# Kernel optimization log

Hardware: AMD Instinct MI355X
Metric: run time of the kernel (lower is better)

Reference implementation:

```python
import jax, jax.numpy as jnp
import numpy as np

RADIUS = 1.3
N_INTR = 128
STEP = 2.0 * RADIUS / N_INTR


def grid_sample_3d(vol, coords):
    # vol: [D,H,W,C]; coords: [N,3] as (x,y,z) in [-1,1]
    # Matches torch grid_sample(align_corners=True, mode='bilinear', padding_mode='border')
    D, H, W, C = vol.shape
    fx = jnp.clip((coords[:, 0] + 1.0) * 0.5 * (W - 1), 0.0, W - 1)
    fy = jnp.clip((coords[:, 1] + 1.0) * 0.5 * (H - 1), 0.0, H - 1)
    fz = jnp.clip((coords[:, 2] + 1.0) * 0.5 * (D - 1), 0.0, D - 1)
    x0 = jnp.floor(fx); y0 = jnp.floor(fy); z0 = jnp.floor(fz)
    wx = fx - x0; wy = fy - y0; wz = fz - z0
    x0i = x0.astype(jnp.int32); y0i = y0.astype(jnp.int32); z0i = z0.astype(jnp.int32)
    x1i = jnp.clip(x0i + 1, 0, W - 1)
    y1i = jnp.clip(y0i + 1, 0, H - 1)
    z1i = jnp.clip(z0i + 1, 0, D - 1)
    out = jnp.zeros((coords.shape[0], C), dtype=vol.dtype)
    for dz in (0, 1):
        iz = z0i if dz == 0 else z1i
        wgtz = (1.0 - wz) if dz == 0 else wz
        for dy in (0, 1):
            iy = y0i if dy == 0 else y1i
            wgty = (1.0 - wy) if dy == 0 else wy
            for dx in (0, 1):
                ix = x0i if dx == 0 else x1i
                wgtx = (1.0 - wx) if dx == 0 else wx
                out = out + vol[iz, iy, ix] * (wgtz * wgty * wgtx)[:, None]
    return out


def sh_deg4(d):
    # tcnn SphericalHarmonics degree 4: input (rd+1)/2, internally mapped back to rd.
    x, y, z = d[:, 0], d[:, 1], d[:, 2]
    x2, y2, z2 = x * x, y * y, z * z
    xy, yz, xz = x * y, y * z, x * z
    return jnp.stack([
        jnp.full_like(x, 0.28209479177387814),
        -0.48860251190291987 * y,
        0.48860251190291987 * z,
        -0.48860251190291987 * x,
        1.0925484305920792 * xy,
        -1.0925484305920792 * yz,
        0.94617469575755997 * z2 - 0.31539156525251999,
        -1.0925484305920792 * xz,
        0.54627421529603959 * (x2 - y2),
        0.59004358992664352 * y * (-3.0 * x2 + y2),
        2.8906114426405538 * xy * z,
        0.45704579946446572 * y * (1.0 - 5.0 * z2),
        0.3731763325901154 * z * (5.0 * z2 - 3.0),
        0.45704579946446572 * x * (1.0 - 5.0 * z2),
        1.4453057213202769 * z * (x2 - y2),
        0.59004358992664352 * x * (-x2 + 3.0 * y2),
    ], axis=-1)


def setup_inputs() -> dict:
    key = jax.random.key(0)
    ks = jax.random.split(key, 10)
    B = 8192
    return {
        'rays_o': jax.random.normal(ks[0], (B, 3), jnp.float32),
        'rays_d': jax.random.normal(ks[1], (B, 3), jnp.float32),
        'G1': 0.01 * jax.random.normal(ks[2], (256, 256, 256, 3), jnp.float32),
        'Fg': 0.05 * jax.random.normal(ks[3], (64, 64, 64, 32), jnp.float32),
        's_w0': 0.05 * jax.random.normal(ks[4], (32, 128), jnp.float32),
        's_w1': 0.05 * jax.random.normal(ks[5], (128, 128), jnp.float32),
        's_w2': 0.05 * jax.random.normal(ks[6], (128, 16), jnp.float32),
        'c_w0': 0.05 * jax.random.normal(ks[7], (31, 64), jnp.float32),
        'c_w1': 0.05 * jax.random.normal(ks[8], (64, 64), jnp.float32),
        'c_w2': 0.05 * jax.random.normal(ks[9], (64, 3), jnp.float32),
    }


def reference(rays_o, rays_d, G1, Fg, s_w0, s_w1, s_w2, c_w0, c_w1, c_w2):
    B = rays_o.shape[0]
    # ray / AABB [-R,R]^3 intersections with uniform stepping
    safe_d = jnp.where(jnp.abs(rays_d) < 1e-9, 1e-9, rays_d)
    t1 = (-RADIUS - rays_o) / safe_d
    t2 = (RADIUS - rays_o) / safe_d
    tmin = jnp.max(jnp.minimum(t1, t2), axis=-1)
    tmax = jnp.min(jnp.maximum(t1, t2), axis=-1)
    tnear = jnp.maximum(tmin, 0.0)
    ts = tnear[:, None] + jnp.arange(N_INTR + 1, dtype=jnp.float32) * STEP  # [B, N+1]
    mask = (ts[:, :-1] < tmax[:, None]) & (tmax > tnear)[:, None]  # [B, N]
    pts = rays_o[:, None, :] + rays_d[:, None, :] * ts[:, :-1, None]  # [B, N, 3]
    # forward scales pts to voxel coords then eval_pts maps back to [-1,1] => pts/RADIUS
    coords = (pts / RADIUS).reshape(-1, 3)
    g1 = grid_sample_3d(G1, coords)                 # [B*N, 3]  chained lookup
    fv = grid_sample_3d(Fg, g1)                     # [B*N, 32]
    h = jax.nn.relu(fv @ s_w0)
    h = jax.nn.relu(h @ s_w1)
    sig_out = h @ s_w2                              # [B*N, 16]
    sigma = jnp.where(mask, jax.nn.relu(sig_out[:, 0].reshape(B, N_INTR)), 0.0)
    dn = rays_d / jnp.linalg.norm(rays_d, axis=-1, keepdims=True)
    enc = sh_deg4(dn)                               # [B, 16]
    enc_pts = jnp.broadcast_to(enc[:, None, :], (B, N_INTR, 16)).reshape(-1, 16)
    cin = jnp.concatenate([enc_pts, sig_out[:, 1:]], axis=-1)  # [B*N, 31]
    ch = jax.nn.relu(cin @ c_w0)
    ch = jax.nn.relu(ch @ c_w1)
    rgb_raw = (ch @ c_w2).reshape(B, N_INTR, 3)
    rgb_raw = jnp.where(mask[..., None], rgb_raw, 0.0)
    # sigma2alpha: delta = step * ||dn|| = step (dn normalized)
    alpha = 1.0 - jnp.exp(-sigma * STEP)
    trans = jnp.cumprod(1.0 - alpha + 1e-10, axis=1)
    trans = jnp.concatenate([jnp.ones((B, 1), alpha.dtype), trans[:, :-1]], axis=1)
    weights = alpha * trans                         # abs_light
    rgb = jnp.sum(weights[..., None] * jax.nn.sigmoid(rgb_raw), axis=1)
    rgb = rgb + (1.0 - jnp.sum(weights, axis=1))[:, None]  # white background
    return rgb
```

## Files before the change

kernel.cpp:

```cpp
#include <hip/hip_runtime.h>
#include <hip/hip_bf16.h>

#define FRADIUS 1.3f
#define FSTEP (2.0f * 1.3f / 128.0f)

typedef __attribute__((ext_vector_type(8))) short short8;
typedef __attribute__((ext_vector_type(16))) float f32x16;

#define MFMA32(a, b, c) __builtin_amdgcn_mfma_f32_32x32x16_bf16((a), (b), (c), 0, 0, 0)

__device__ __forceinline__ unsigned pk2(float a, float b) {
    __hip_bfloat162 hh = __float22bfloat162_rn(make_float2(a, b));
    union { __hip_bfloat162 h; unsigned u; } cv;
    cv.h = hh;
    return cv.u;
}

__device__ __forceinline__ void ray_aabb(float ox, float oy, float oz,
                                         float dx, float dy, float dz,
                                         float& tnear, float& tmax) {
    float sdx = (fabsf(dx) < 1e-9f) ? 1e-9f : dx;
    float sdy = (fabsf(dy) < 1e-9f) ? 1e-9f : dy;
    float sdz = (fabsf(dz) < 1e-9f) ? 1e-9f : dz;
    float t1x = (-FRADIUS - ox) / sdx, t2x = (FRADIUS - ox) / sdx;
    float t1y = (-FRADIUS - oy) / sdy, t2y = (FRADIUS - oy) / sdy;
    float t1z = (-FRADIUS - oz) / sdz, t2z = (FRADIUS - oz) / sdz;
    float tmin = fmaxf(fmaxf(fminf(t1x, t2x), fminf(t1y, t2y)), fminf(t1z, t2z));
    tmax = fminf(fminf(fmaxf(t1x, t2x), fmaxf(t1y, t2y)), fmaxf(t1z, t2z));
    tnear = fmaxf(tmin, 0.0f);
}

__global__ void prep_weights_kernel(const float* __restrict__ s_w0, const float* __restrict__ s_w1,
                                    const float* __restrict__ s_w2, const float* __restrict__ c_w0,
                                    const float* __restrict__ c_w1, const float* __restrict__ c_w2,
                                    uint4* __restrict__ ws) {
    int fid = blockIdx.x;
    int l = threadIdx.x;
    int h = l >> 5, m = l & 31;
    int layer, nt = 0, kt = 0;
    if (fid < 8)       { layer = 0; nt = fid >> 1; kt = fid & 1; }
    else if (fid < 40) { layer = 1; int f = fid - 8;  nt = f >> 3; kt = f & 7; }
    else if (fid < 48) { layer = 2; kt = fid - 40; }
    else if (fid < 52) { layer = 3; int f = fid - 48; nt = f >> 1; kt = f & 1; }
    else if (fid < 60) { layer = 4; int f = fid - 52; nt = f >> 2; kt = f & 3; }
    else               { layer = 5; kt = fid - 60; }
    int n = nt * 32 + m;
    float v[8];
#pragma unroll
    for (int j = 0; j < 8; ++j) {
        int k = kt * 16 + h * 8 + j;
        float x;
        if (layer == 0)      x = s_w0[k * 128 + n];
        else if (layer == 1) x = s_w1[k * 128 + n];
        else if (layer == 2) x = (n < 16) ? s_w2[k * 16 + n] : 0.0f;
        else if (layer == 3) x = (k < 16) ? c_w0[k * 64 + n]
                                 : ((k == 16) ? 0.0f : c_w0[(k - 1) * 64 + n]);
        else if (layer == 4) x = c_w1[k * 64 + n];
        else                 x = (n < 3) ? c_w2[k * 3 + n] : 0.0f;
        v[j] = x;
    }
    uint4 u;
    u.x = pk2(v[0], v[1]); u.y = pk2(v[2], v[3]);
    u.z = pk2(v[4], v[5]); u.w = pk2(v[6], v[7]);
    ws[fid * 64 + l] = u;
}

__global__ __launch_bounds__(256) void sample_kernel(
    const float* __restrict__ rays_o, const float* __restrict__ rays_d,
    const float* __restrict__ G1, const float* __restrict__ Fg,
    uint4* __restrict__ fvout) {
    const int idx = blockIdx.x * 256 + threadIdx.x;
    const int ray = idx >> 7;
    const int s = idx & 127;

    const float ox = rays_o[ray * 3 + 0], oy = rays_o[ray * 3 + 1], oz = rays_o[ray * 3 + 2];
    const float dx = rays_d[ray * 3 + 0], dy = rays_d[ray * 3 + 1], dz = rays_d[ray * 3 + 2];

    float tnear, tmax;
    ray_aabb(ox, oy, oz, dx, dy, dz, tnear, tmax);
    float t = tnear + (float)s * FSTEP;
    bool maskb = (t < tmax) && (tmax > tnear);

    uint4* op = fvout + (size_t)(idx >> 5) * 128 + (idx & 31);
    if (!maskb) {
        uint4 z = {0u, 0u, 0u, 0u};
#pragma unroll
        for (int q = 0; q < 4; ++q) op[q * 32] = z;
        return;
    }

    float px = ox + dx * t, py = oy + dy * t, pz = oz + dz * t;
    const float invR = 1.0f / FRADIUS;
    float cx = px * invR, cy = py * invR, cz = pz * invR;

    float fx = fminf(fmaxf((cx + 1.0f) * 0.5f * 255.0f, 0.0f), 255.0f);
    float fy = fminf(fmaxf((cy + 1.0f) * 0.5f * 255.0f, 0.0f), 255.0f);
    float fz = fminf(fmaxf((cz + 1.0f) * 0.5f * 255.0f, 0.0f), 255.0f);
    float x0f = floorf(fx), y0f = floorf(fy), z0f = floorf(fz);
    float wx = fx - x0f, wy = fy - y0f, wz = fz - z0f;
    int x0 = (int)x0f, y0 = (int)y0f, z0 = (int)z0f;
    int x1 = min(x0 + 1, 255), y1 = min(y0 + 1, 255), z1 = min(z0 + 1, 255);
    float g1x = 0.f, g1y = 0.f, g1z = 0.f;
    {
        float wz0 = 1.f - wz, wy0 = 1.f - wy, wx0 = 1.f - wx;
#pragma unroll
        for (int cc = 0; cc < 8; ++cc) {
            int zz = (cc & 4) ? z1 : z0;
            int yy = (cc & 2) ? y1 : y0;
            int xx = (cc & 1) ? x1 : x0;
            float wgt = ((cc & 4) ? wz : wz0) * ((cc & 2) ? wy : wy0) * ((cc & 1) ? wx : wx0);
            int gidx = (((zz << 8) | yy) << 8 | xx) * 3;
            g1x = fmaf(wgt, G1[gidx + 0], g1x);
            g1y = fmaf(wgt, G1[gidx + 1], g1y);
            g1z = fmaf(wgt, G1[gidx + 2], g1z);
        }
    }

    float4 fvv[8];
#pragma unroll
    for (int q = 0; q < 8; ++q) fvv[q] = make_float4(0.f, 0.f, 0.f, 0.f);
    {
        float gfx = fminf(fmaxf((g1x + 1.0f) * 0.5f * 63.0f, 0.0f), 63.0f);
        float gfy = fminf(fmaxf((g1y + 1.0f) * 0.5f * 63.0f, 0.0f), 63.0f);
        float gfz = fminf(fmaxf((g1z + 1.0f) * 0.5f * 63.0f, 0.0f), 63.0f);
        float gx0f = floorf(gfx), gy0f = floorf(gfy), gz0f = floorf(gfz);
        float gwx = gfx - gx0f, gwy = gfy - gy0f, gwz = gfz - gz0f;
        int gx0 = (int)gx0f, gy0 = (int)gy0f, gz0 = (int)gz0f;
        int gx1 = min(gx0 + 1, 63), gy1 = min(gy0 + 1, 63), gz1 = min(gz0 + 1, 63);
        float wz0 = 1.f - gwz, wy0 = 1.f - gwy, wx0 = 1.f - gwx;
#pragma unroll
        for (int cc = 0; cc < 8; ++cc) {
            int zz = (cc & 4) ? gz1 : gz0;
            int yy = (cc & 2) ? gy1 : gy0;
            int xx = (cc & 1) ? gx1 : gx0;
            float wgt = ((cc & 4) ? gwz : wz0) * ((cc & 2) ? gwy : wy0) * ((cc & 1) ? gwx : wx0);
            const float4* p = (const float4*)(Fg + (((((zz << 6) | yy) << 6) | xx) << 5));
#pragma unroll
            for (int q = 0; q < 8; ++q) {
                float4 v = p[q];
                fvv[q].x = fmaf(wgt, v.x, fvv[q].x);
                fvv[q].y = fmaf(wgt, v.y, fvv[q].y);
                fvv[q].z = fmaf(wgt, v.z, fvv[q].z);
                fvv[q].w = fmaf(wgt, v.w, fvv[q].w);
            }
        }
    }

#pragma unroll
    for (int q = 0; q < 4; ++q) {
        uint4 u;
        u.x = pk2(fvv[2 * q].x, fvv[2 * q].y);
        u.y = pk2(fvv[2 * q].z, fvv[2 * q].w);
        u.z = pk2(fvv[2 * q + 1].x, fvv[2 * q + 1].y);
        u.w = pk2(fvv[2 * q + 1].z, fvv[2 * q + 1].w);
        op[q * 32] = u;
    }
}

#define BUILD_B(B, PK, BASE) do {                                         \
    unsigned own0 = h ? (PK)[(BASE) + 2] : (PK)[(BASE) + 0];              \
    unsigned own1 = h ? (PK)[(BASE) + 3] : (PK)[(BASE) + 1];              \
    unsigned snd0 = h ? (PK)[(BASE) + 0] : (PK)[(BASE) + 2];              \
    unsigned snd1 = h ? (PK)[(BASE) + 1] : (PK)[(BASE) + 3];              \
    unsigned r0 = (unsigned)__shfl_xor((int)snd0, 32, 64);                \
    unsigned r1 = (unsigned)__shfl_xor((int)snd1, 32, 64);                \
    union { unsigned u[4]; short8 v; } bb;                                \
    bb.u[0] = h ? r0 : own0;  bb.u[1] = h ? r1 : own1;                    \
    bb.u[2] = h ? own0 : r0;  bb.u[3] = h ? own1 : r1;                    \
    (B) = bb.v; } while (0)

__global__ __launch_bounds__(512, 4) void mlp_kernel6(
    const float* __restrict__ rays_o, const float* __restrict__ rays_d,
    const uint4* __restrict__ wsg, const short8* __restrict__ fvin,
    float* __restrict__ out) {

    __shared__ uint4 wlds[64 * 64];
    __shared__ float4 comp[2][128];

    const int tid = threadIdx.x;
    const int w = tid >> 6;
    const int lane = tid & 63;
    const int h = lane >> 5;
    const int c = lane & 31;
    const int wr = w >> 2;
    const int chunk = w & 3;
    const int ray = blockIdx.x * 2 + wr;
    const int cbase = chunk * 32;

#pragma unroll
    for (int i = 0; i < 8; ++i) wlds[tid + i * 512] = wsg[tid + i * 512];
    __syncthreads();

    const float ox = rays_o[ray * 3 + 0], oy = rays_o[ray * 3 + 1], oz = rays_o[ray * 3 + 2];
    const float dx = rays_d[ray * 3 + 0], dy = rays_d[ray * 3 + 1], dz = rays_d[ray * 3 + 2];

    float tnear, tmax;
    ray_aabb(ox, oy, oz, dx, dy, dz, tnear, tmax);
    const bool hit = (tmax > tnear);
    const bool dead = !hit || (tnear + (float)cbase * FSTEP >= tmax);

    if (dead) {
        if (lane < 32) comp[wr][cbase + lane] = make_float4(0.f, 0.f, 0.f, 0.f);
    } else {
        const f32x16 z16 = {0.f};

        unsigned p0[32];
        {
            short8 xb[2];
            const int g = ray * 4 + chunk;
#pragma unroll
            for (int kt = 0; kt < 2; ++kt)
                xb[kt] = fvin[(size_t)g * 128 + (kt * 2 + h) * 32 + c];
#pragma unroll
            for (int nt = 0; nt < 4; ++nt) {
                f32x16 a = z16;
#pragma unroll
                for (int kt = 0; kt < 2; ++kt) {
                    short8 wv = *(const short8*)&wlds[(nt * 2 + kt) * 64 + lane];
                    a = MFMA32(wv, xb[kt], a);
                }
#pragma unroll
                for (int p = 0; p < 8; ++p)
                    p0[nt * 8 + p] = pk2(fmaxf(a[2 * p], 0.f), fmaxf(a[2 * p + 1], 0.f));
            }
        }

        unsigned p1[32];
#pragma unroll
        for (int nt = 0; nt < 4; ++nt) {
            f32x16 a = z16;
#pragma unroll
            for (int kt = 0; kt < 8; ++kt) {
                short8 B0;
                BUILD_B(B0, p0, 4 * kt);
                short8 wv = *(const short8*)&wlds[(8 + nt * 8 + kt) * 64 + lane];
                a = MFMA32(wv, B0, a);
            }
#pragma unroll
            for (int p = 0; p < 8; ++p)
                p1[nt * 8 + p] = pk2(fmaxf(a[2 * p], 0.f), fmaxf(a[2 * p + 1], 0.f));
        }

        unsigned s2p[4];
        float alphaR;
        {
            f32x16 S = z16;
#pragma unroll
            for (int kt = 0; kt < 8; ++kt) {
                short8 B0;
                BUILD_B(B0, p1, 4 * kt);
                short8 wv = *(const short8*)&wlds[(40 + kt) * 64 + lane];
                S = MFMA32(wv, B0, S);
            }
#pragma unroll
            for (int p = 0; p < 4; ++p) s2p[p] = pk2(S[2 * p], S[2 * p + 1]);
            float tp = tnear + (float)(cbase + c) * FSTEP;
            float sg = fmaxf(S[0], 0.f);
            alphaR = (tp < tmax) ? 1.0f - __expf(-sg * FSTEP) : 0.0f;
        }

        short8 Benc;
        {
            float inv = rsqrtf(dx * dx + dy * dy + dz * dz);
            float nx = dx * inv, ny = dy * inv, nz = dz * inv;
            float nx2 = nx * nx, ny2 = ny * ny, nz2 = nz * nz;
            float nxy = nx * ny, nyz = ny * nz, nxz = nx * nz;
            float e0 = 0.28209479177387814f;
            float e1 = -0.48860251190291987f * ny;
            float e2 = 0.48860251190291987f * nz;
            float e3 = -0.48860251190291987f * nx;
            float e4 = 1.0925484305920792f * nxy;
            float e5 = -1.0925484305920792f * nyz;
            float e6 = 0.94617469575756f * nz2 - 0.31539156525252f;
            float e7 = -1.0925484305920792f * nxz;
            float e8 = 0.5462742152960396f * (nx2 - ny2);
            float e9 = 0.5900435899266435f * ny * (-3.0f * nx2 + ny2);
            float e10 = 2.890611442640554f * nxy * nz;
            float e11 = 0.4570457994644657f * ny * (1.0f - 5.0f * nz2);
            float e12 = 0.3731763325901154f * nz * (5.0f * nz2 - 3.0f);
            float e13 = 0.4570457994644657f * nx * (1.0f - 5.0f * nz2);
            float e14 = 1.445305721320277f * nz * (nx2 - ny2);
            float e15 = 0.5900435899266435f * nx * (-nx2 + 3.0f * ny2);
            union { unsigned u[4]; short8 v; } bb;
            bb.u[0] = h ? pk2(e8, e9)   : pk2(e0, e1);
            bb.u[1] = h ? pk2(e10, e11) : pk2(e2, e3);
            bb.u[2] = h ? pk2(e12, e13) : pk2(e4, e5);
            bb.u[3] = h ? pk2(e14, e15) : pk2(e6, e7);
            Benc = bb.v;
        }

        unsigned c0p[16];
        {
            short8 Bs0;
            BUILD_B(Bs0, s2p, 0);
#pragma unroll
            for (int nt = 0; nt < 2; ++nt) {
                f32x16 a = z16;
                short8 wv0 = *(const short8*)&wlds[(48 + nt * 2 + 0) * 64 + lane];
                a = MFMA32(wv0, Benc, a);
                short8 wv1 = *(const short8*)&wlds[(48 + nt * 2 + 1) * 64 + lane];
                a = MFMA32(wv1, Bs0, a);
#pragma unroll
                for (int p = 0; p < 8; ++p)
                    c0p[nt * 8 + p] = pk2(fmaxf(a[2 * p], 0.f), fmaxf(a[2 * p + 1], 0.f));
            }
        }

        unsigned c1p[16];
#pragma unroll
        for (int nt = 0; nt < 2; ++nt) {
            f32x16 a = z16;
#pragma unroll
            for (int kt = 0; kt < 4; ++kt) {
                short8 B0;
                BUILD_B(B0, c0p, 4 * kt);
                short8 wv = *(const short8*)&wlds[(52 + nt * 4 + kt) * 64 + lane];
                a = MFMA32(wv, B0, a);
            }
#pragma unroll
            for (int p = 0; p < 8; ++p)
                c1p[nt * 8 + p] = pk2(fmaxf(a[2 * p], 0.f), fmaxf(a[2 * p + 1], 0.f));
        }

        {
            f32x16 F = z16;
#pragma unroll
            for (int kt = 0; kt < 4; ++kt) {
                short8 B0;
                BUILD_B(B0, c1p, 4 * kt);
                short8 wv = *(const short8*)&wlds[(60 + kt) * 64 + lane];
                F = MFMA32(wv, B0, F);
            }
            if (h == 0) {
                float4 cv;
                cv.x = alphaR;
                cv.y = 1.0f / (1.0f + __expf(-F[0]));
                cv.z = 1.0f / (1.0f + __expf(-F[1]));
                cv.w = 1.0f / (1.0f + __expf(-F[2]));
                comp[wr][cbase + c] = cv;
            }
        }
    }

    __syncthreads();

    if (tid < 128) {
        const int cr = tid >> 6;
        const int ln = tid & 63;
        float4 vl = comp[cr][ln];
        float4 vh = comp[cr][ln + 64];
        float a_lo = vl.x, a_hi = vh.x;
        float m_lo = 1.0f - a_lo + 1e-10f;
        float m_hi = 1.0f - a_hi + 1e-10f;

        float p = m_lo;
#pragma unroll
        for (int off = 1; off < 64; off <<= 1) {
            float q = __shfl_up(p, off, 64);
            if (ln >= off) p *= q;
        }
        float ph = m_hi;
#pragma unroll
        for (int off = 1; off < 64; off <<= 1) {
            float q = __shfl_up(ph, off, 64);
            if (ln >= off) ph *= q;
        }
        float total_lo = __shfl(p, 63, 64);
        float e_lo = __shfl_up(p, 1, 64);
        if (ln == 0) e_lo = 1.0f;
        float e_hi = __shfl_up(ph, 1, 64);
        if (ln == 0) e_hi = 1.0f;
        e_hi *= total_lo;

        float w_lo = a_lo * e_lo;
        float w_hi = a_hi * e_hi;

        float sr = w_lo * vl.y + w_hi * vh.y;
        float sg = w_lo * vl.z + w_hi * vh.z;
        float sb = w_lo * vl.w + w_hi * vh.w;
        float sw = w_lo + w_hi;
#pragma unroll
        for (int off = 32; off >= 1; off >>= 1) {
            sr += __shfl_xor(sr, off, 64);
            sg += __shfl_xor(sg, off, 64);
            sb += __shfl_xor(sb, off, 64);
            sw += __shfl_xor(sw, off, 64);
        }
        if (ln == 0) {
            int rg = blockIdx.x * 2 + cr;
            float bg = 1.0f - sw;
            out[rg * 3 + 0] = sr + bg;
            out[rg * 3 + 1] = sg + bg;
            out[rg * 3 + 2] = sb + bg;
        }
    }
}

extern "C" void kernel_launch(void* const* d_in, const int* in_sizes, int n_in,
                              void* d_out, int out_size, void* d_ws, size_t ws_size,
                              hipStream_t stream) {
    const float* rays_o = (const float*)d_in[0];
    const float* rays_d = (const float*)d_in[1];
    const float* G1 = (const float*)d_in[2];
    const float* Fg = (const float*)d_in[3];
    const float* s_w0 = (const float*)d_in[4];
    const float* s_w1 = (const float*)d_in[5];
    const float* s_w2 = (const float*)d_in[6];
    const float* c_w0 = (const float*)d_in[7];
    const float* c_w1 = (const float*)d_in[8];
    const float* c_w2 = (const float*)d_in[9];
    float* out = (float*)d_out;

    const int B = in_sizes[0] / 3;
    const int npts = B * 128;

    const size_t FV_OFF = 65536;
    const size_t need = FV_OFF + (size_t)npts * 64;
    if (ws_size < need) return;

    uint4* fv = (uint4*)((char*)d_ws + FV_OFF);

    prep_weights_kernel<<<dim3(64), dim3(64), 0, stream>>>(s_w0, s_w1, s_w2, c_w0, c_w1, c_w2,
                                                           (uint4*)d_ws);
    sample_kernel<<<dim3(npts / 256), dim3(256), 0, stream>>>(rays_o, rays_d, G1, Fg, fv);
    mlp_kernel6<<<dim3(B / 2), dim3(512), 0, stream>>>(rays_o, rays_d, (const uint4*)d_ws,
                                                       (const short8*)fv, out);
}
```

Measured before the change: 108.6 us.

## Fuse grid sampling into MLP kernel via shared-memory feature buffer

Merges the sampling kernel into the MLP kernel. The first 256 threads of each block compute the 256 sample features for the block's two rays and write bf16 features to LDS, while the other 256 threads load the weights into LDS. This removes the global write and reread of the feature buffer and one kernel launch. To stay within the LDS budget, the weights for the last two color layers are now read from global memory, and the sampling work runs on only half of each block's threads, which may lower occupancy or add latency.

```diff
diff --git a/kernel.cpp b/kernel.cpp
--- a/kernel.cpp
+++ b/kernel.cpp
@@ -65,98 +65,6 @@
     ws[fid * 64 + l] = u;
 }
 
-__global__ __launch_bounds__(256) void sample_kernel(
-    const float* __restrict__ rays_o, const float* __restrict__ rays_d,
-    const float* __restrict__ G1, const float* __restrict__ Fg,
-    uint4* __restrict__ fvout) {
-    const int idx = blockIdx.x * 256 + threadIdx.x;
-    const int ray = idx >> 7;
-    const int s = idx & 127;
-
-    const float ox = rays_o[ray * 3 + 0], oy = rays_o[ray * 3 + 1], oz = rays_o[ray * 3 + 2];
-    const float dx = rays_d[ray * 3 + 0], dy = rays_d[ray * 3 + 1], dz = rays_d[ray * 3 + 2];
-
-    float tnear, tmax;
-    ray_aabb(ox, oy, oz, dx, dy, dz, tnear, tmax);
-    float t = tnear + (float)s * FSTEP;
-    bool maskb = (t < tmax) && (tmax > tnear);
-
-    uint4* op = fvout + (size_t)(idx >> 5) * 128 + (idx & 31);
-    if (!maskb) {
-        uint4 z = {0u, 0u, 0u, 0u};
-#pragma unroll
-        for (int q = 0; q < 4; ++q) op[q * 32] = z;
-        return;
-    }
-
-    float px = ox + dx * t, py = oy + dy * t, pz = oz + dz * t;
-    const float invR = 1.0f / FRADIUS;
-    float cx = px * invR, cy = py * invR, cz = pz * invR;
-
-    float fx = fminf(fmaxf((cx + 1.0f) * 0.5f * 255.0f, 0.0f), 255.0f);
-    float fy = fminf(fmaxf((cy + 1.0f) * 0.5f * 255.0f, 0.0f), 255.0f);
-    float fz = fminf(fmaxf((cz + 1.0f) * 0.5f * 255.0f, 0.0f), 255.0f);
-    float x0f = floorf(fx), y0f = floorf(fy), z0f = floorf(fz);
-    float wx = fx - x0f, wy = fy - y0f, wz = fz - z0f;
-    int x0 = (int)x0f, y0 = (int)y0f, z0 = (int)z0f;
-    int x1 = min(x0 + 1, 255), y1 = min(y0 + 1, 255), z1 = min(z0 + 1, 255);
-    float g1x = 0.f, g1y = 0.f, g1z = 0.f;
-    {
-        float wz0 = 1.f - wz, wy0 = 1.f - wy, wx0 = 1.f - wx;
-#pragma unroll
-        for (int cc = 0; cc < 8; ++cc) {
-            int zz = (cc & 4) ? z1 : z0;
-            int yy = (cc & 2) ? y1 : y0;
-            int xx = (cc & 1) ? x1 : x0;
-            float wgt = ((cc & 4) ? wz : wz0) * ((cc & 2) ? wy : wy0) * ((cc & 1) ? wx : wx0);
-            int gidx = (((zz << 8) | yy) << 8 | xx) * 3;
-            g1x = fmaf(wgt, G1[gidx + 0], g1x);
-            g1y = fmaf(wgt, G1[gidx + 1], g1y);
-            g1z = fmaf(wgt, G1[gidx + 2], g1z);
-        }
-    }
-
-    float4 fvv[8];
-#pragma unroll
-    for (int q = 0; q < 8; ++q) fvv[q] = make_float4(0.f, 0.f, 0.f, 0.f);
-    {
-        float gfx = fminf(fmaxf((g1x + 1.0f) * 0.5f * 63.0f, 0.0f), 63.0f);
-        float gfy = fminf(fmaxf((g1y + 1.0f) * 0.5f * 63.0f, 0.0f), 63.0f);
-        float gfz = fminf(fmaxf((g1z + 1.0f) * 0.5f * 63.0f, 0.0f), 63.0f);
-        float gx0f = floorf(gfx), gy0f = floorf(gfy), gz0f = floorf(gfz);
-        float gwx = gfx - gx0f, gwy = gfy - gy0f, gwz = gfz - gz0f;
-        int gx0 = (int)gx0f, gy0 = (int)gy0f, gz0 = (int)gz0f;
-        int gx1 = min(gx0 + 1, 63), gy1 = min(gy0 + 1, 63), gz1 = min(gz0 + 1, 63);
-        float wz0 = 1.f - gwz, wy0 = 1.f - gwy, wx0 = 1.f - gwx;
-#pragma unroll
-        for (int cc = 0; cc < 8; ++cc) {
-            int zz = (cc & 4) ? gz1 : gz0;
-            int yy = (cc & 2) ? gy1 : gy0;
-            int xx = (cc & 1) ? gx1 : gx0;
-            float wgt = ((cc & 4) ? gwz : wz0) * ((cc & 2) ? gwy : wy0) * ((cc & 1) ? gwx : wx0);
-            const float4* p = (const float4*)(Fg + (((((zz << 6) | yy) << 6) | xx) << 5));
-#pragma unroll
-            for (int q = 0; q < 8; ++q) {
-                float4 v = p[q];
-                fvv[q].x = fmaf(wgt, v.x, fvv[q].x);
-                fvv[q].y = fmaf(wgt, v.y, fvv[q].y);
-                fvv[q].z = fmaf(wgt, v.z, fvv[q].z);
-                fvv[q].w = fmaf(wgt, v.w, fvv[q].w);
-            }
-        }
-    }
-
-#pragma unroll
-    for (int q = 0; q < 4; ++q) {
-        uint4 u;
-        u.x = pk2(fvv[2 * q].x, fvv[2 * q].y);
-        u.y = pk2(fvv[2 * q].z, fvv[2 * q].w);
-        u.z = pk2(fvv[2 * q + 1].x, fvv[2 * q + 1].y);
-        u.w = pk2(fvv[2 * q + 1].z, fvv[2 * q + 1].w);
-        op[q * 32] = u;
-    }
-}
-
 #define BUILD_B(B, PK, BASE) do {                                         \
     unsigned own0 = h ? (PK)[(BASE) + 2] : (PK)[(BASE) + 0];              \
     unsigned own1 = h ? (PK)[(BASE) + 3] : (PK)[(BASE) + 1];              \
@@ -169,12 +77,13 @@
     bb.u[2] = h ? own0 : r0;  bb.u[3] = h ? own1 : r1;                    \
     (B) = bb.v; } while (0)
 
-__global__ __launch_bounds__(512, 4) void mlp_kernel6(
+__global__ __launch_bounds__(512, 4) void fused_kernel(
     const float* __restrict__ rays_o, const float* __restrict__ rays_d,
-    const uint4* __restrict__ wsg, const short8* __restrict__ fvin,
-    float* __restrict__ out) {
-
-    __shared__ uint4 wlds[64 * 64];
+    const float* __restrict__ G1, const float* __restrict__ Fg,
+    const uint4* __restrict__ wsg, float* __restrict__ out) {
+
+    __shared__ uint4 wlds[52 * 64];
+    __shared__ uint4 fvb[8 * 4 * 32];
     __shared__ float4 comp[2][128];
 
     const int tid = threadIdx.x;
@@ -187,8 +96,97 @@
     const int ray = blockIdx.x * 2 + wr;
     const int cbase = chunk * 32;
 
-#pragma unroll
-    for (int i = 0; i < 8; ++i) wlds[tid + i * 512] = wsg[tid + i * 512];
+    if (tid < 256) {
+        const int idx = blockIdx.x * 256 + tid;
+        const int gray = idx >> 7;
+        const int s = idx & 127;
+
+        const float ox = rays_o[gray * 3 + 0], oy = rays_o[gray * 3 + 1], oz = rays_o[gray * 3 + 2];
+        const float dx = rays_d[gray * 3 + 0], dy = rays_d[gray * 3 + 1], dz = rays_d[gray * 3 + 2];
+
+        float tnear, tmax;
+        ray_aabb(ox, oy, oz, dx, dy, dz, tnear, tmax);
+        float t = tnear + (float)s * FSTEP;
+        bool maskb = (t < tmax) && (tmax > tnear);
+
+        uint4* op = &fvb[(tid >> 5) * 128 + (tid & 31)];
+        if (!maskb) {
+            uint4 z = {0u, 0u, 0u, 0u};
+#pragma unroll
+            for (int q = 0; q < 4; ++q) op[q * 32] = z;
+        } else {
+            float px = ox + dx * t, py = oy + dy * t, pz = oz + dz * t;
+            const float invR = 1.0f / FRADIUS;
+            float cx = px * invR, cy = py * invR, cz = pz * invR;
+
+            float fx = fminf(fmaxf((cx + 1.0f) * 0.5f * 255.0f, 0.0f), 255.0f);
+            float fy = fminf(fmaxf((cy + 1.0f) * 0.5f * 255.0f, 0.0f), 255.0f);
+            float fz = fminf(fmaxf((cz + 1.0f) * 0.5f * 255.0f, 0.0f), 255.0f);
+            float x0f = floorf(fx), y0f = floorf(fy), z0f = floorf(fz);
+            float wx = fx - x0f, wy = fy - y0f, wz = fz - z0f;
+            int x0 = (int)x0f, y0 = (int)y0f, z0 = (int)z0f;
+            int x1 = min(x0 + 1, 255), y1 = min(y0 + 1, 255), z1 = min(z0 + 1, 255);
+            float g1x = 0.f, g1y = 0.f, g1z = 0.f;
+            {
+                float wz0 = 1.f - wz, wy0 = 1.f - wy, wx0 = 1.f - wx;
+#pragma unroll
+                for (int cc = 0; cc < 8; ++cc) {
+                    int zz = (cc & 4) ? z1 : z0;
+                    int yy = (cc & 2) ? y1 : y0;
+                    int xx = (cc & 1) ? x1 : x0;
+                    float wgt = ((cc & 4) ? wz : wz0) * ((cc & 2) ? wy : wy0) * ((cc & 1) ? wx : wx0);
+                    int gidx = (((zz << 8) | yy) << 8 | xx) * 3;
+                    g1x = fmaf(wgt, G1[gidx + 0], g1x);
+                    g1y = fmaf(wgt, G1[gidx + 1], g1y);
+                    g1z = fmaf(wgt, G1[gidx + 2], g1z);
+                }
+            }
+
+            float4 fvv[8];
+#pragma unroll
+            for (int q = 0; q < 8; ++q) fvv[q] = make_float4(0.f, 0.f, 0.f, 0.f);
+            {
+                float gfx = fminf(fmaxf((g1x + 1.0f) * 0.5f * 63.0f, 0.0f), 63.0f);
+                float gfy = fminf(fmaxf((g1y + 1.0f) * 0.5f * 63.0f, 0.0f), 63.0f);
+                float gfz = fminf(fmaxf((g1z + 1.0f) * 0.5f * 63.0f, 0.0f), 63.0f);
+                float gx0f = floorf(gfx), gy0f = floorf(gfy), gz0f = floorf(gfz);
+                float gwx = gfx - gx0f, gwy = gfy - gy0f, gwz = gfz - gz0f;
+                int gx0 = (int)gx0f, gy0 = (int)gy0f, gz0 = (int)gz0f;
+                int gx1 = min(gx0 + 1, 63), gy1 = min(gy0 + 1, 63), gz1 = min(gz0 + 1, 63);
+                float wz0 = 1.f - gwz, wy0 = 1.f - gwy, wx0 = 1.f - gwx;
+#pragma unroll
+                for (int cc = 0; cc < 8; ++cc) {
+                    int zz = (cc & 4) ? gz1 : gz0;
+                    int yy = (cc & 2) ? gy1 : gy0;
+                    int xx = (cc & 1) ? gx1 : gx0;
+                    float wgt = ((cc & 4) ? gwz : wz0) * ((cc & 2) ? gwy : wy0) * ((cc & 1) ? gwx : wx0);
+                    const float4* p = (const float4*)(Fg + (((((zz << 6) | yy) << 6) | xx) << 5));
+#pragma unroll
+                    for (int q = 0; q < 8; ++q) {
+                        float4 v = p[q];
+                        fvv[q].x = fmaf(wgt, v.x, fvv[q].x);
+                        fvv[q].y = fmaf(wgt, v.y, fvv[q].y);
+                        fvv[q].z = fmaf(wgt, v.z, fvv[q].z);
+                        fvv[q].w = fmaf(wgt, v.w, fvv[q].w);
+                    }
+                }
+            }
+
+#pragma unroll
+            for (int q = 0; q < 4; ++q) {
+                uint4 u;
+                u.x = pk2(fvv[2 * q].x, fvv[2 * q].y);
+                u.y = pk2(fvv[2 * q].z, fvv[2 * q].w);
+                u.z = pk2(fvv[2 * q + 1].x, fvv[2 * q + 1].y);
+                u.w = pk2(fvv[2 * q + 1].z, fvv[2 * q + 1].w);
+                op[q * 32] = u;
+            }
+        }
+    } else {
+        const int t = tid - 256;
+#pragma unroll
+        for (int i = 0; i < 13; ++i) wlds[t + i * 256] = wsg[t + i * 256];
+    }
     __syncthreads();
 
     const float ox = rays_o[ray * 3 + 0], oy = rays_o[ray * 3 + 1], oz = rays_o[ray * 3 + 2];
@@ -207,10 +205,9 @@
         unsigned p0[32];
         {
             short8 xb[2];
-            const int g = ray * 4 + chunk;
 #pragma unroll
             for (int kt = 0; kt < 2; ++kt)
-                xb[kt] = fvin[(size_t)g * 128 + (kt * 2 + h) * 32 + c];
+                xb[kt] = *(const short8*)&fvb[w * 128 + (kt * 2 + h) * 32 + c];
 #pragma unroll
             for (int nt = 0; nt < 4; ++nt) {
                 f32x16 a = z16;
@@ -314,7 +311,7 @@
             for (int kt = 0; kt < 4; ++kt) {
                 short8 B0;
                 BUILD_B(B0, c0p, 4 * kt);
-                short8 wv = *(const short8*)&wlds[(52 + nt * 4 + kt) * 64 + lane];
+                short8 wv = *(const short8*)&wsg[(52 + nt * 4 + kt) * 64 + lane];
                 a = MFMA32(wv, B0, a);
             }
 #pragma unroll
@@ -328,7 +325,7 @@
             for (int kt = 0; kt < 4; ++kt) {
                 short8 B0;
                 BUILD_B(B0, c1p, 4 * kt);
-                short8 wv = *(const short8*)&wlds[(60 + kt) * 64 + lane];
+                short8 wv = *(const short8*)&wsg[(60 + kt) * 64 + lane];
                 F = MFMA32(wv, B0, F);
             }
             if (h == 0) {
@@ -412,17 +409,11 @@
     float* out = (float*)d_out;
 
     const int B = in_sizes[0] / 3;
-    const int npts = B * 128;
-
-    const size_t FV_OFF = 65536;
-    const size_t need = FV_OFF + (size_t)npts * 64;
-    if (ws_size < need) return;
-
-    uint4* fv = (uint4*)((char*)d_ws + FV_OFF);
+
+    if (ws_size < 65536) return;
 
     prep_weights_kernel<<<dim3(64), dim3(64), 0, stream>>>(s_w0, s_w1, s_w2, c_w0, c_w1, c_w2,
                                                            (uint4*)d_ws);
-    sample_kernel<<<dim3(npts / 256), dim3(256), 0, stream>>>(rays_o, rays_d, G1, Fg, fv);
-    mlp_kernel6<<<dim3(B / 2), dim3(512), 0, stream>>>(rays_o, rays_d, (const uint4*)d_ws,
-                                                       (const short8*)fv, out);
+    fused_kernel<<<dim3(B / 2), dim3(512), 0, stream>>>(rays_o, rays_d, G1, Fg,
+                                                        (const uint4*)d_ws, out);
 }
```

Result: no change. 110.7 us (+2.0%).

## Switch MLP path to FP8 scaled MFMA with 64-deep K tiles

Applied to the files above, without the earlier changes.

Replaces the bf16 32x32x16 MFMA chain with the scaled FP8 32x32x64 MFMA, quantizing weights, grid features and activations to fp8 with power-of-two prescaling and compensating scale factors. This cuts the MFMA instruction count by about four, halves the intermediate feature buffer traffic and shrinks the weight LDS footprint. Feature layout is changed to a contiguous per-point 32-byte record. It risks accuracy loss from fp8 quantization of activations and weights, and half the lanes feed zero padding when K is below 64.

```diff
diff --git a/kernel.cpp b/kernel.cpp
--- a/kernel.cpp
+++ b/kernel.cpp
@@ -4,16 +4,16 @@
 #define FRADIUS 1.3f
 #define FSTEP (2.0f * 1.3f / 128.0f)
 
-typedef __attribute__((ext_vector_type(8))) short short8;
+typedef __attribute__((ext_vector_type(8))) int int8v;
 typedef __attribute__((ext_vector_type(16))) float f32x16;
 
-#define MFMA32(a, b, c) __builtin_amdgcn_mfma_f32_32x32x16_bf16((a), (b), (c), 0, 0, 0)
-
-__device__ __forceinline__ unsigned pk2(float a, float b) {
-    __hip_bfloat162 hh = __float22bfloat162_rn(make_float2(a, b));
-    union { __hip_bfloat162 h; unsigned u; } cv;
-    cv.h = hh;
-    return cv.u;
+#define MFMAS(a, b, c) \
+    __builtin_amdgcn_mfma_scale_f32_32x32x64_f8f6f4((a), (b), (c), 0, 0, 0, 121, 0, 127)
+
+__device__ __forceinline__ unsigned pkf8(float a, float b, float c2, float d) {
+    int t = __builtin_amdgcn_cvt_pk_fp8_f32(a, b, 0, false);
+    t = __builtin_amdgcn_cvt_pk_fp8_f32(c2, d, t, true);
+    return (unsigned)t;
 }
 
 __device__ __forceinline__ void ray_aabb(float ox, float oy, float oz,
@@ -34,35 +34,41 @@
                                     const float* __restrict__ s_w2, const float* __restrict__ c_w0,
                                     const float* __restrict__ c_w1, const float* __restrict__ c_w2,
                                     uint4* __restrict__ ws) {
-    int fid = blockIdx.x;
-    int l = threadIdx.x;
-    int h = l >> 5, m = l & 31;
-    int layer, nt = 0, kt = 0;
-    if (fid < 8)       { layer = 0; nt = fid >> 1; kt = fid & 1; }
-    else if (fid < 40) { layer = 1; int f = fid - 8;  nt = f >> 3; kt = f & 7; }
-    else if (fid < 48) { layer = 2; kt = fid - 40; }
-    else if (fid < 52) { layer = 3; int f = fid - 48; nt = f >> 1; kt = f & 1; }
-    else if (fid < 60) { layer = 4; int f = fid - 52; nt = f >> 2; kt = f & 3; }
-    else               { layer = 5; kt = fid - 60; }
-    int n = nt * 32 + m;
-    float v[8];
-#pragma unroll
-    for (int j = 0; j < 8; ++j) {
-        int k = kt * 16 + h * 8 + j;
-        float x;
-        if (layer == 0)      x = s_w0[k * 128 + n];
-        else if (layer == 1) x = s_w1[k * 128 + n];
-        else if (layer == 2) x = (n < 16) ? s_w2[k * 16 + n] : 0.0f;
-        else if (layer == 3) x = (k < 16) ? c_w0[k * 64 + n]
-                                 : ((k == 16) ? 0.0f : c_w0[(k - 1) * 64 + n]);
-        else if (layer == 4) x = c_w1[k * 64 + n];
-        else                 x = (n < 3) ? c_w2[k * 3 + n] : 0.0f;
-        v[j] = x;
-    }
-    uint4 u;
-    u.x = pk2(v[0], v[1]); u.y = pk2(v[2], v[3]);
-    u.z = pk2(v[4], v[5]); u.w = pk2(v[6], v[7]);
-    ws[fid * 64 + l] = u;
+    const int fid = blockIdx.x;
+    const int l = threadIdx.x;
+    const int hA = l >> 5, m = l & 31;
+    float v[32];
+#pragma unroll
+    for (int j = 0; j < 32; ++j) {
+        const int kl = hA * 32 + j;
+        float x = 0.0f;
+        if (fid < 4) {
+            if (kl < 32) x = s_w0[kl * 128 + fid * 32 + m];
+        } else if (fid < 12) {
+            int t = fid - 4, nt = t >> 1, kt = t & 1;
+            x = s_w1[(kt * 64 + kl) * 128 + nt * 32 + m];
+        } else if (fid < 14) {
+            int kt = fid - 12;
+            if (m < 16) x = s_w2[(kt * 64 + kl) * 16 + m];
+        } else if (fid < 16) {
+            int nt = fid - 14;
+            if (kl < 16) x = c_w0[kl * 64 + nt * 32 + m];
+            else if (kl > 16 && kl < 32) x = c_w0[(kl - 1) * 64 + nt * 32 + m];
+        } else if (fid < 18) {
+            int nt = fid - 16;
+            x = c_w1[kl * 64 + nt * 32 + m];
+        } else {
+            if (m < 3) x = c_w2[kl * 3 + m];
+        }
+        v[j] = 64.0f * x;
+    }
+    uint4 lo, hi;
+    lo.x = pkf8(v[0], v[1], v[2], v[3]);    lo.y = pkf8(v[4], v[5], v[6], v[7]);
+    lo.z = pkf8(v[8], v[9], v[10], v[11]);  lo.w = pkf8(v[12], v[13], v[14], v[15]);
+    hi.x = pkf8(v[16], v[17], v[18], v[19]); hi.y = pkf8(v[20], v[21], v[22], v[23]);
+    hi.z = pkf8(v[24], v[25], v[26], v[27]); hi.w = pkf8(v[28], v[29], v[30], v[31]);
+    ws[fid * 128 + l] = lo;
+    ws[fid * 128 + 64 + l] = hi;
 }
 
 __global__ __launch_bounds__(256) void sample_kernel(
@@ -81,11 +87,10 @@
     float t = tnear + (float)s * FSTEP;
     bool maskb = (t < tmax) && (tmax > tnear);
 
-    uint4* op = fvout + (size_t)(idx >> 5) * 128 + (idx & 31);
+    uint4* op = fvout + (size_t)idx * 2;
     if (!maskb) {
         uint4 z = {0u, 0u, 0u, 0u};
-#pragma unroll
-        for (int q = 0; q < 4; ++q) op[q * 32] = z;
+        op[0] = z; op[1] = z;
         return;
     }
 
@@ -133,7 +138,8 @@
             int zz = (cc & 4) ? gz1 : gz0;
             int yy = (cc & 2) ? gy1 : gy0;
             int xx = (cc & 1) ? gx1 : gx0;
-            float wgt = ((cc & 4) ? gwz : wz0) * ((cc & 2) ? gwy : wy0) * ((cc & 1) ? gwx : wx0);
+            float wgt = 256.0f * ((cc & 4) ? gwz : wz0) * ((cc & 2) ? gwy : wy0) *
+                        ((cc & 1) ? gwx : wx0);
             const float4* p = (const float4*)(Fg + (((((zz << 6) | yy) << 6) | xx) << 5));
 #pragma unroll
             for (int q = 0; q < 8; ++q) {
@@ -146,35 +152,43 @@
         }
     }
 
-#pragma unroll
-    for (int q = 0; q < 4; ++q) {
-        uint4 u;
-        u.x = pk2(fvv[2 * q].x, fvv[2 * q].y);
-        u.y = pk2(fvv[2 * q].z, fvv[2 * q].w);
-        u.z = pk2(fvv[2 * q + 1].x, fvv[2 * q + 1].y);
-        u.w = pk2(fvv[2 * q + 1].z, fvv[2 * q + 1].w);
-        op[q * 32] = u;
-    }
-}
-
-#define BUILD_B(B, PK, BASE) do {                                         \
-    unsigned own0 = h ? (PK)[(BASE) + 2] : (PK)[(BASE) + 0];              \
-    unsigned own1 = h ? (PK)[(BASE) + 3] : (PK)[(BASE) + 1];              \
-    unsigned snd0 = h ? (PK)[(BASE) + 0] : (PK)[(BASE) + 2];              \
-    unsigned snd1 = h ? (PK)[(BASE) + 1] : (PK)[(BASE) + 3];              \
-    unsigned r0 = (unsigned)__shfl_xor((int)snd0, 32, 64);                \
-    unsigned r1 = (unsigned)__shfl_xor((int)snd1, 32, 64);                \
-    union { unsigned u[4]; short8 v; } bb;                                \
-    bb.u[0] = h ? r0 : own0;  bb.u[1] = h ? r1 : own1;                    \
-    bb.u[2] = h ? own0 : r0;  bb.u[3] = h ? own1 : r1;                    \
-    (B) = bb.v; } while (0)
-
-__global__ __launch_bounds__(512, 4) void mlp_kernel6(
+    uint4 lo, hi;
+    lo.x = pkf8(fvv[0].x, fvv[0].y, fvv[0].z, fvv[0].w);
+    lo.y = pkf8(fvv[1].x, fvv[1].y, fvv[1].z, fvv[1].w);
+    lo.z = pkf8(fvv[2].x, fvv[2].y, fvv[2].z, fvv[2].w);
+    lo.w = pkf8(fvv[3].x, fvv[3].y, fvv[3].z, fvv[3].w);
+    hi.x = pkf8(fvv[4].x, fvv[4].y, fvv[4].z, fvv[4].w);
+    hi.y = pkf8(fvv[5].x, fvv[5].y, fvv[5].z, fvv[5].w);
+    hi.z = pkf8(fvv[6].x, fvv[6].y, fvv[6].z, fvv[6].w);
+    hi.w = pkf8(fvv[7].x, fvv[7].y, fvv[7].z, fvv[7].w);
+    op[0] = lo; op[1] = hi;
+}
+
+#define PACKR(dst, a) do {                                                              \
+    (dst)[0] = pkf8(fmaxf((a)[0], 0.f), fmaxf((a)[1], 0.f), fmaxf((a)[2], 0.f), fmaxf((a)[3], 0.f)); \
+    (dst)[1] = pkf8(fmaxf((a)[4], 0.f), fmaxf((a)[5], 0.f), fmaxf((a)[6], 0.f), fmaxf((a)[7], 0.f)); \
+    (dst)[2] = pkf8(fmaxf((a)[8], 0.f), fmaxf((a)[9], 0.f), fmaxf((a)[10], 0.f), fmaxf((a)[11], 0.f)); \
+    (dst)[3] = pkf8(fmaxf((a)[12], 0.f), fmaxf((a)[13], 0.f), fmaxf((a)[14], 0.f), fmaxf((a)[15], 0.f)); \
+} while (0)
+
+#define BUILD2(B, TA, TB) do {                                                          \
+    union { unsigned u[8]; int8v v; } bb_;                                              \
+    _Pragma("unroll")                                                                   \
+    for (int q_ = 0; q_ < 4; ++q_) {                                                    \
+        unsigned snd_ = h ? (TA)[q_] : (TB)[q_];                                        \
+        unsigned rec_ = (unsigned)__shfl_xor((int)snd_, 32, 64);                        \
+        unsigned own_ = h ? (TB)[q_] : (TA)[q_];                                        \
+        bb_.u[2 * q_]     = h ? rec_ : own_;                                            \
+        bb_.u[2 * q_ + 1] = h ? own_ : rec_;                                            \
+    }                                                                                   \
+    (B) = bb_.v; } while (0)
+
+__global__ __launch_bounds__(512, 4) void mlp_fp8_kernel(
     const float* __restrict__ rays_o, const float* __restrict__ rays_d,
-    const uint4* __restrict__ wsg, const short8* __restrict__ fvin,
+    const uint4* __restrict__ wsg, const uint4* __restrict__ fvin,
     float* __restrict__ out) {
 
-    __shared__ uint4 wlds[64 * 64];
+    __shared__ uint4 wlds[19 * 128];
     __shared__ float4 comp[2][128];
 
     const int tid = threadIdx.x;
@@ -188,7 +202,10 @@
     const int cbase = chunk * 32;
 
 #pragma unroll
-    for (int i = 0; i < 8; ++i) wlds[tid + i * 512] = wsg[tid + i * 512];
+    for (int i = 0; i < 5; ++i) {
+        int tt = tid + i * 512;
+        if (tt < 19 * 128) wlds[tt] = wsg[tt];
+    }
     __syncthreads();
 
     const float ox = rays_o[ray * 3 + 0], oy = rays_o[ray * 3 + 1], oz = rays_o[ray * 3 + 2];
@@ -204,139 +221,128 @@
     } else {
         const f32x16 z16 = {0.f};
 
-        unsigned p0[32];
+        auto AF = [&](int f) -> int8v {
+            union { uint4 u4[2]; int8v v; } t;
+            t.u4[0] = wlds[f * 128 + lane];
+            t.u4[1] = wlds[f * 128 + 64 + lane];
+            return t.v;
+        };
+
+        int8v xb;
         {
-            short8 xb[2];
-            const int g = ray * 4 + chunk;
-#pragma unroll
-            for (int kt = 0; kt < 2; ++kt)
-                xb[kt] = fvin[(size_t)g * 128 + (kt * 2 + h) * 32 + c];
-#pragma unroll
-            for (int nt = 0; nt < 4; ++nt) {
-                f32x16 a = z16;
-#pragma unroll
-                for (int kt = 0; kt < 2; ++kt) {
-                    short8 wv = *(const short8*)&wlds[(nt * 2 + kt) * 64 + lane];
-                    a = MFMA32(wv, xb[kt], a);
-                }
-#pragma unroll
-                for (int p = 0; p < 8; ++p)
-                    p0[nt * 8 + p] = pk2(fmaxf(a[2 * p], 0.f), fmaxf(a[2 * p + 1], 0.f));
+            union { uint4 u4[2]; int8v v; } bb;
+            uint4 z = {0u, 0u, 0u, 0u};
+            if (h == 0) {
+                size_t p = (size_t)(ray * 128 + cbase + c) * 2;
+                bb.u4[0] = fvin[p];
+                bb.u4[1] = fvin[p + 1];
+            } else {
+                bb.u4[0] = z; bb.u4[1] = z;
             }
-        }
-
-        unsigned p1[32];
+            xb = bb.v;
+        }
+
+        unsigned o0[4][4];
 #pragma unroll
         for (int nt = 0; nt < 4; ++nt) {
-            f32x16 a = z16;
-#pragma unroll
-            for (int kt = 0; kt < 8; ++kt) {
-                short8 B0;
-                BUILD_B(B0, p0, 4 * kt);
-                short8 wv = *(const short8*)&wlds[(8 + nt * 8 + kt) * 64 + lane];
-                a = MFMA32(wv, B0, a);
-            }
-#pragma unroll
-            for (int p = 0; p < 8; ++p)
-                p1[nt * 8 + p] = pk2(fmaxf(a[2 * p], 0.f), fmaxf(a[2 * p + 1], 0.f));
-        }
-
-        unsigned s2p[4];
+            f32x16 a = MFMAS(AF(nt), xb, z16);
+            PACKR(o0[nt], a);
+        }
+        int8v b0k0, b0k1;
+        BUILD2(b0k0, o0[0], o0[1]);
+        BUILD2(b0k1, o0[2], o0[3]);
+
+        unsigned o1[4][4];
+#pragma unroll
+        for (int nt = 0; nt < 4; ++nt) {
+            f32x16 a = MFMAS(AF(4 + nt * 2 + 0), b0k0, z16);
+            a = MFMAS(AF(4 + nt * 2 + 1), b0k1, a);
+            PACKR(o1[nt], a);
+        }
+        int8v b1k0, b1k1;
+        BUILD2(b1k0, o1[0], o1[1]);
+        BUILD2(b1k1, o1[2], o1[3]);
+
+        f32x16 S = MFMAS(AF(12), b1k0, z16);
+        S = MFMAS(AF(13), b1k1, S);
+        unsigned os2[2];
+        os2[0] = pkf8(S[0], S[1], S[2], S[3]);
+        os2[1] = pkf8(S[4], S[5], S[6], S[7]);
         float alphaR;
         {
-            f32x16 S = z16;
-#pragma unroll
-            for (int kt = 0; kt < 8; ++kt) {
-                short8 B0;
-                BUILD_B(B0, p1, 4 * kt);
-                short8 wv = *(const short8*)&wlds[(40 + kt) * 64 + lane];
-                S = MFMA32(wv, B0, S);
+            float tp = tnear + (float)(cbase + c) * FSTEP;
+            float sg = fmaxf(S[0], 0.f) * (1.0f / 256.0f);
+            alphaR = (tp < tmax) ? 1.0f - __expf(-sg * FSTEP) : 0.0f;
+        }
+
+        int8v bc;
+        {
+            unsigned rec0 = (unsigned)__shfl_xor((int)os2[0], 32, 64);
+            unsigned rec1 = (unsigned)__shfl_xor((int)os2[1], 32, 64);
+            union { unsigned u[8]; int8v v; } bb;
+            if (h == 0) {
+                float inv = rsqrtf(dx * dx + dy * dy + dz * dz);
+                float nx = dx * inv, ny = dy * inv, nz = dz * inv;
+                float nx2 = nx * nx, ny2 = ny * ny, nz2 = nz * nz;
+                float nxy = nx * ny, nyz = ny * nz, nxz = nx * nz;
+                float e0 = 256.0f * 0.28209479177387814f;
+                float e1 = 256.0f * -0.48860251190291987f * ny;
+                float e2 = 256.0f * 0.48860251190291987f * nz;
+                float e3 = 256.0f * -0.48860251190291987f * nx;
+                float e4 = 256.0f * 1.0925484305920792f * nxy;
+                float e5 = 256.0f * -1.0925484305920792f * nyz;
+                float e6 = 256.0f * (0.94617469575756f * nz2 - 0.31539156525252f);
+                float e7 = 256.0f * -1.0925484305920792f * nxz;
+                float e8 = 256.0f * 0.5462742152960396f * (nx2 - ny2);
+                float e9 = 256.0f * 0.5900435899266435f * ny * (-3.0f * nx2 + ny2);
+                float e10 = 256.0f * 2.890611442640554f * nxy * nz;
+                float e11 = 256.0f * 0.4570457994644657f * ny * (1.0f - 5.0f * nz2);
+                float e12 = 256.0f * 0.3731763325901154f * nz * (5.0f * nz2 - 3.0f);
+                float e13 = 256.0f * 0.4570457994644657f * nx * (1.0f - 5.0f * nz2);
+                float e14 = 256.0f * 1.445305721320277f * nz * (nx2 - ny2);
+                float e15 = 256.0f * 0.5900435899266435f * nx * (-nx2 + 3.0f * ny2);
+                bb.u[0] = pkf8(e0, e1, e2, e3);
+                bb.u[1] = pkf8(e4, e5, e6, e7);
+                bb.u[2] = pkf8(e8, e9, e10, e11);
+                bb.u[3] = pkf8(e12, e13, e14, e15);
+                bb.u[4] = os2[0] & 0xFFFFFF00u;
+                bb.u[5] = rec0;
+                bb.u[6] = os2[1];
+                bb.u[7] = rec1;
+            } else {
+#pragma unroll
+                for (int q = 0; q < 8; ++q) bb.u[q] = 0u;
             }
-#pragma unroll
-            for (int p = 0; p < 4; ++p) s2p[p] = pk2(S[2 * p], S[2 * p + 1]);
-            float tp = tnear + (float)(cbase + c) * FSTEP;
-            float sg = fmaxf(S[0], 0.f);
-            alphaR = (tp < tmax) ? 1.0f - __expf(-sg * FSTEP) : 0.0f;
-        }
-
-        short8 Benc;
+            bc = bb.v;
+        }
+
+        unsigned oc0[2][4];
+#pragma unroll
+        for (int nt = 0; nt < 2; ++nt) {
+            f32x16 a = MFMAS(AF(14 + nt), bc, z16);
+            PACKR(oc0[nt], a);
+        }
+        int8v bcc;
+        BUILD2(bcc, oc0[0], oc0[1]);
+
+        unsigned oc1[2][4];
+#pragma unroll
+        for (int nt = 0; nt < 2; ++nt) {
+            f32x16 a = MFMAS(AF(16 + nt), bcc, z16);
+            PACKR(oc1[nt], a);
+        }
+        int8v bd;
+        BUILD2(bd, oc1[0], oc1[1]);
+
         {
-            float inv = rsqrtf(dx * dx + dy * dy + dz * dz);
-            float nx = dx * inv, ny = dy * inv, nz = dz * inv;
-            float nx2 = nx * nx, ny2 = ny * ny, nz2 = nz * nz;
-            float nxy = nx * ny, nyz = ny * nz, nxz = nx * nz;
-            float e0 = 0.28209479177387814f;
-            float e1 = -0.48860251190291987f * ny;
-            float e2 = 0.48860251190291987f * nz;
-            float e3 = -0.48860251190291987f * nx;
-            float e4 = 1.0925484305920792f * nxy;
-            float e5 = -1.0925484305920792f * nyz;
-            float e6 = 0.94617469575756f * nz2 - 0.31539156525252f;
-            float e7 = -1.0925484305920792f * nxz;
-            float e8 = 0.5462742152960396f * (nx2 - ny2);
-            float e9 = 0.5900435899266435f * ny * (-3.0f * nx2 + ny2);
-            float e10 = 2.890611442640554f * nxy * nz;
-            float e11 = 0.4570457994644657f * ny * (1.0f - 5.0f * nz2);
-            float e12 = 0.3731763325901154f * nz * (5.0f * nz2 - 3.0f);
-            float e13 = 0.4570457994644657f * nx * (1.0f - 5.0f * nz2);
-            float e14 = 1.445305721320277f * nz * (nx2 - ny2);
-            float e15 = 0.5900435899266435f * nx * (-nx2 + 3.0f * ny2);
-            union { unsigned u[4]; short8 v; } bb;
-            bb.u[0] = h ? pk2(e8, e9)   : pk2(e0, e1);
-            bb.u[1] = h ? pk2(e10, e11) : pk2(e2, e3);
-            bb.u[2] = h ? pk2(e12, e13) : pk2(e4, e5);
-            bb.u[3] = h ? pk2(e14, e15) : pk2(e6, e7);
-            Benc = bb.v;
-        }
-
-        unsigned c0p[16];
-        {
-            short8 Bs0;
-            BUILD_B(Bs0, s2p, 0);
-#pragma unroll
-            for (int nt = 0; nt < 2; ++nt) {
-                f32x16 a = z16;
-                short8 wv0 = *(const short8*)&wlds[(48 + nt * 2 + 0) * 64 + lane];
-                a = MFMA32(wv0, Benc, a);
-                short8 wv1 = *(const short8*)&wlds[(48 + nt * 2 + 1) * 64 + lane];
-                a = MFMA32(wv1, Bs0, a);
-#pragma unroll
-                for (int p = 0; p < 8; ++p)
-                    c0p[nt * 8 + p] = pk2(fmaxf(a[2 * p], 0.f), fmaxf(a[2 * p + 1], 0.f));
-            }
-        }
-
-        unsigned c1p[16];
-#pragma unroll
-        for (int nt = 0; nt < 2; ++nt) {
-            f32x16 a = z16;
-#pragma unroll
-            for (int kt = 0; kt < 4; ++kt) {
-                short8 B0;
-                BUILD_B(B0, c0p, 4 * kt);
-                short8 wv = *(const short8*)&wlds[(52 + nt * 4 + kt) * 64 + lane];
-                a = MFMA32(wv, B0, a);
-            }
-#pragma unroll
-            for (int p = 0; p < 8; ++p)
-                c1p[nt * 8 + p] = pk2(fmaxf(a[2 * p], 0.f), fmaxf(a[2 * p + 1], 0.f));
-        }
-
-        {
-            f32x16 F = z16;
-#pragma unroll
-            for (int kt = 0; kt < 4; ++kt) {
-                short8 B0;
-                BUILD_B(B0, c1p, 4 * kt);
-                short8 wv = *(const short8*)&wlds[(60 + kt) * 64 + lane];
-                F = MFMA32(wv, B0, F);
-            }
+            f32x16 F = MFMAS(AF(18), bd, z16);
             if (h == 0) {
+                const float s8 = 1.0f / 256.0f;
                 float4 cv;
                 cv.x = alphaR;
-                cv.y = 1.0f / (1.0f + __expf(-F[0]));
-                cv.z = 1.0f / (1.0f + __expf(-F[1]));
-                cv.w = 1.0f / (1.0f + __expf(-F[2]));
+                cv.y = 1.0f / (1.0f + __expf(-F[0] * s8));
+                cv.z = 1.0f / (1.0f + __expf(-F[1] * s8));
+                cv.w = 1.0f / (1.0f + __expf(-F[2] * s8));
                 comp[wr][cbase + c] = cv;
             }
         }
@@ -415,14 +421,14 @@
     const int npts = B * 128;
 
     const size_t FV_OFF = 65536;
-    const size_t need = FV_OFF + (size_t)npts * 64;
+    const size_t need = FV_OFF + (size_t)npts * 32;
     if (ws_size < need) return;
 
     uint4* fv = (uint4*)((char*)d_ws + FV_OFF);
 
-    prep_weights_kernel<<<dim3(64), dim3(64), 0, stream>>>(s_w0, s_w1, s_w2, c_w0, c_w1, c_w2,
+    prep_weights_kernel<<<dim3(19), dim3(64), 0, stream>>>(s_w0, s_w1, s_w2, c_w0, c_w1, c_w2,
                                                            (uint4*)d_ws);
     sample_kernel<<<dim3(npts / 256), dim3(256), 0, stream>>>(rays_o, rays_d, G1, Fg, fv);
-    mlp_kernel6<<<dim3(B / 2), dim3(512), 0, stream>>>(rays_o, rays_d, (const uint4*)d_ws,
-                                                       (const short8*)fv, out);
-}
+    mlp_fp8_kernel<<<dim3(B / 2), dim3(512), 0, stream>>>(rays_o, rays_d, (const uint4*)d_ws,
+                                                          fv, out);
+}
```

After: 90.58 us, median of 2. 1.2x faster.
